# Optimization experiments

Measured on AMD Instinct MI355X. Metric: run time of the kernel, lower is better.

The kernel has to match this reference:

```python
import jax, jax.numpy as jnp
import numpy as np

LMAX = 3
NUM_IRREPS = (LMAX + 1) ** 2  # 16
# Allowed CG paths (l1, l2, l3): triangle inequality, l3 <= LMAX, parity-even (Gaunt-nonzero)
PATHS = tuple((l1, l2, l3)
              for l1 in range(LMAX + 1)
              for l2 in range(LMAX + 1)
              for l3 in range(abs(l1 - l2), min(l1 + l2, LMAX) + 1)
              if (l1 + l2 + l3) % 2 == 0)
NUM_PATHS = len(PATHS)  # 23


def _sph_harm(v, xp):
    """Real spherical harmonics up to l=3 for unit vectors v[..., 3] -> [..., 16]."""
    x, y, z = v[..., 0], v[..., 1], v[..., 2]
    x2, y2, z2 = x * x, y * y, z * z
    Y = [xp.full_like(x, 0.28209479177387814),
         0.4886025119029199 * y, 0.4886025119029199 * z, 0.4886025119029199 * x,
         1.0925484305920792 * x * y, 1.0925484305920792 * y * z,
         0.31539156525252005 * (3.0 * z2 - 1.0),
         1.0925484305920792 * x * z, 0.5462742152960396 * (x2 - y2),
         0.5900435899266435 * y * (3.0 * x2 - y2), 2.890611442640554 * x * y * z,
         0.4570457994644658 * y * (5.0 * z2 - 1.0), 0.3731763325901154 * z * (5.0 * z2 - 3.0),
         0.4570457994644658 * x * (5.0 * z2 - 1.0), 1.445305721320277 * z * (x2 - y2),
         0.5900435899266435 * x * (x2 - 3.0 * y2)]
    return xp.stack(Y, axis=-1)


def _gaunt_coeffs():
    """Gaunt coefficients C[i,j,k] = integral Y_i Y_j Y_k dOmega via exact quadrature."""
    nodes, w = np.polynomial.legendre.leggauss(16)  # cos(theta), exact to deg 31
    nphi = 32
    phi = (np.arange(nphi) + 0.5) * (2.0 * np.pi / nphi)
    ct = nodes[:, None]
    st = np.sqrt(1.0 - ct ** 2)
    dirs = np.stack([st * np.cos(phi), st * np.sin(phi),
                     np.broadcast_to(ct, (16, nphi))], axis=-1).reshape(-1, 3)
    ww = (w[:, None] * np.full((1, nphi), 2.0 * np.pi / nphi)).reshape(-1)
    Y = _sph_harm(dirs, np)  # [M, 16]
    C = np.einsum('m,mi,mj,mk->ijk', ww, Y, Y, Y)
    return C.astype(np.float32)


def setup_inputs() -> dict:
    key = jax.random.key(0)
    k1, k2, k3, k4, k5 = jax.random.split(key, 5)
    N_ATOMS, N_EDGES, HIDDEN, OUT = 20000, 100000, 64, 64
    node_features = jax.random.normal(k1, (N_ATOMS, HIDDEN, NUM_IRREPS), dtype=jnp.float32)
    ev = jax.random.normal(k2, (N_EDGES, 3), dtype=jnp.float32)
    edge_vectors = ev / jnp.linalg.norm(ev, axis=-1, keepdims=True)  # unit directions
    edge_index = jax.random.randint(k3, (2, N_EDGES), 0, N_ATOMS, dtype=jnp.int32)
    cg = jnp.asarray(_gaunt_coeffs())  # [16, 16, 16]
    tp_weights = jax.random.normal(k4, (NUM_PATHS, HIDDEN, OUT), dtype=jnp.float32) / np.sqrt(HIDDEN)
    W_lin = jax.random.normal(k5, (OUT, OUT * NUM_IRREPS), dtype=jnp.float32) / np.sqrt(OUT * NUM_IRREPS)
    b_lin = jnp.zeros((OUT,), dtype=jnp.float32)
    return {"node_features": node_features, "edge_vectors": edge_vectors,
            "edge_index": edge_index, "cg": cg, "tp_weights": tp_weights,
            "W_lin": W_lin, "b_lin": b_lin}


def reference(node_features, edge_vectors, edge_index, cg, tp_weights, W_lin, b_lin):
    n_atoms = node_features.shape[0]
    n_edges = edge_vectors.shape[0]
    out_ch = tp_weights.shape[2]
    Y = _sph_harm(edge_vectors, jnp)                       # [E, 16]
    src = node_features[edge_index[0]]                     # gather: [E, H, 16]
    msgs = jnp.zeros((n_edges, out_ch, NUM_IRREPS), node_features.dtype)
    for p, (l1, l2, l3) in enumerate(PATHS):               # fixed 23-path structural loop
        s1 = slice(l1 * l1, (l1 + 1) ** 2)
        s2 = slice(l2 * l2, (l2 + 1) ** 2)
        s3 = slice(l3 * l3, (l3 + 1) ** 2)
        # CG contraction of node irrep l1 with SH irrep l2 into output irrep l3
        u = jnp.einsum('ehi,ej,ijk->ehk', src[:, :, s1], Y[:, s2], cg[s1, s2, s3])
        msgs = msgs.at[:, :, s3].add(jnp.einsum('ehk,ho->eok', u, tp_weights[p]))
    agg = jax.ops.segment_sum(msgs, edge_index[1], num_segments=n_atoms)  # scatter-add [N, O, 16]
    flat = agg.reshape(n_atoms, -1)
    return flat @ W_lin.T + b_lin
```

## Files before the change

### kernel.cpp

```cpp
#include <hip/hip_runtime.h>


#define NKK 99
#define NKPAD 112
#define EPB 32
#define THREADS 256
#define SA_ESTR 516
#define SU_HSTR 40
#define SU_ESTR 648
#define RED_ESTR 68

typedef _Float16 f16;
typedef f16 f16x4 __attribute__((ext_vector_type(4)));
typedef f16 f16x8 __attribute__((ext_vector_type(8)));
typedef float f32x4 __attribute__((ext_vector_type(4)));

__device__ __constant__ short PK_P[NKK] = {
  0, 1,1,1, 2,2,2,2,2, 3,3,3,3,3,3,3, 4,4,4, 5, 6,6,6,6,6, 7,7,7,
  8,8,8,8,8,8,8, 9,9,9,9,9, 10,10,10,10,10, 11,11,11, 12,12,12,12,12,12,12,
  13, 14,14,14,14,14, 15,15,15, 16,16,16,16,16,16,16, 17,17,17,17,17,17,17,
  18,18,18,18,18, 19,19,19, 20,20,20,20,20,20,20, 21, 22,22,22,22,22};
__device__ __constant__ short KK_L1[NKK] = {
  0, 0,0,0, 0,0,0,0,0, 0,0,0,0,0,0,0, 1,1,1, 1, 1,1,1,1,1, 1,1,1,
  1,1,1,1,1,1,1, 1,1,1,1,1, 2,2,2,2,2, 2,2,2, 2,2,2,2,2,2,2,
  2, 2,2,2,2,2, 2,2,2, 2,2,2,2,2,2,2, 3,3,3,3,3,3,3,
  3,3,3,3,3, 3,3,3, 3,3,3,3,3,3,3, 3, 3,3,3,3,3};
__device__ __constant__ short KK_L2[NKK] = {
  0, 1,1,1, 2,2,2,2,2, 3,3,3,3,3,3,3, 0,0,0, 1, 1,1,1,1,1, 2,2,2,
  2,2,2,2,2,2,2, 3,3,3,3,3, 0,0,0,0,0, 1,1,1, 1,1,1,1,1,1,1,
  2, 2,2,2,2,2, 3,3,3, 3,3,3,3,3,3,3, 0,0,0,0,0,0,0,
  1,1,1,1,1, 2,2,2, 2,2,2,2,2,2,2, 3, 3,3,3,3,3};
__device__ __constant__ short KK_KG[NKK] = {
  0, 1,2,3, 4,5,6,7,8, 9,10,11,12,13,14,15, 1,2,3, 0, 4,5,6,7,8, 1,2,3,
  9,10,11,12,13,14,15, 4,5,6,7,8, 4,5,6,7,8, 1,2,3, 9,10,11,12,13,14,15,
  0, 4,5,6,7,8, 1,2,3, 9,10,11,12,13,14,15, 9,10,11,12,13,14,15,
  4,5,6,7,8, 1,2,3, 9,10,11,12,13,14,15, 0, 4,5,6,7,8};

__global__ __launch_bounds__(256) void compute_F(const float* __restrict__ tpw,
                                                 const float* __restrict__ wlin,
                                                 const float* __restrict__ cg,
                                                 f16* __restrict__ F,
                                                 f16* __restrict__ CGd) {
  int kk = blockIdx.x;
  int tid = threadIdx.x;

  {
    int i = tid >> 4, j = tid & 15;
    f16 v = (f16)0.f;
    if (kk < NKK) {
      int l1 = KK_L1[kk], l2 = KK_L2[kk], kg = KK_KG[kk];
      int b1 = l1 * l1, b2 = l2 * l2;
      if (i >= b1 && i < b1 + 2 * l1 + 1 && j >= b2 && j < b2 + 2 * l2 + 1)
        v = (f16)cg[(i * 16 + j) * 16 + kg];
    }
    CGd[kk * 256 + tid] = v;
  }

  if (kk >= NKK) {
    for (int r = tid; r < 64 * 64; r += 256) F[(size_t)r * NKPAD + kk] = (f16)0.f;
    return;
  }
  int p  = PK_P[kk];
  int c3 = KK_KG[kk];

  __shared__ float wl[64][65];
  for (int idx = tid; idx < 64 * 64; idx += 256) {
    int o2 = idx >> 6, o = idx & 63;
    wl[o2][o] = wlin[o2 * 1024 + o * 16 + c3];
  }
  __syncthreads();

  int h = tid & 63, og = tid >> 6;
  float acc[16];
#pragma unroll
  for (int m = 0; m < 16; ++m) acc[m] = 0.f;
  const float* tw = tpw + (p * 64 + h) * 64;
  for (int o = 0; o < 64; ++o) {
    float w = tw[o];
#pragma unroll
    for (int m = 0; m < 16; ++m) acc[m] += w * wl[og * 16 + m][o];
  }
#pragma unroll
  for (int m = 0; m < 16; ++m)
    F[(size_t)(h * 64 + og * 16 + m) * NKPAD + kk] = (f16)acc[m];
}

__global__ void init_out(float* __restrict__ out, const float* __restrict__ b, int n) {
  int i = blockIdx.x * 256 + threadIdx.x;
  if (i < n) out[i] = b[i & 63];
}

__global__ __launch_bounds__(THREADS, 2) void edge_kernel(
    const float* __restrict__ nf, const float* __restrict__ ev,
    const int* __restrict__ eidx, const f16* __restrict__ CGd,
    const f16* __restrict__ F, float* __restrict__ out, int NE) {

  __shared__ f16 sYh[EPB * 16];
  __shared__ int sSrcA[EPB];
  __shared__ int sDst[EPB];
  __shared__ f16 sA[EPB * SA_ESTR];
  __shared__ f16 sU[EPB * SU_ESTR];

  int tid = threadIdx.x;
  int wave = tid >> 6, lane = tid & 63;
  int lm = lane & 15, lq = lane >> 4;

  if (tid < EPB) {
    int eg = blockIdx.x * EPB + tid;
    int sa = 0, da = -1;
    float x = 0.f, y = 0.f, z = 0.f;
    if (eg < NE) {
      sa = eidx[eg];
      da = eidx[NE + eg];
      x = ev[3 * eg + 0]; y = ev[3 * eg + 1]; z = ev[3 * eg + 2];
    }
    sSrcA[tid] = sa;
    sDst[tid] = da;
    float x2 = x * x, y2 = y * y, z2 = z * z;
    float Y[16];
    Y[0]  = 0.28209479177387814f;
    Y[1]  = 0.4886025119029199f * y;
    Y[2]  = 0.4886025119029199f * z;
    Y[3]  = 0.4886025119029199f * x;
    Y[4]  = 1.0925484305920792f * x * y;
    Y[5]  = 1.0925484305920792f * y * z;
    Y[6]  = 0.31539156525252005f * (3.0f * z2 - 1.0f);
    Y[7]  = 1.0925484305920792f * x * z;
    Y[8]  = 0.5462742152960396f * (x2 - y2);
    Y[9]  = 0.5900435899266435f * y * (3.0f * x2 - y2);
    Y[10] = 2.890611442640554f * x * y * z;
    Y[11] = 0.4570457994644658f * y * (5.0f * z2 - 1.0f);
    Y[12] = 0.3731763325901154f * z * (5.0f * z2 - 3.0f);
    Y[13] = 0.4570457994644658f * x * (5.0f * z2 - 1.0f);
    Y[14] = 1.445305721320277f  * z * (x2 - y2);
    Y[15] = 0.5900435899266435f * x * (x2 - 3.0f * y2);
#pragma unroll
    for (int j = 0; j < 16; ++j) sYh[tid * 16 + j] = (f16)Y[j];
  }
  __syncthreads();

  f16x4 Sf[8][4];
  int ebase = wave * 8;
#pragma unroll
  for (int ei = 0; ei < 8; ++ei) {
    const float4* src4 = (const float4*)nf + (size_t)sSrcA[ebase + ei] * 256;
#pragma unroll
    for (int hg = 0; hg < 4; ++hg) {
      float4 v = src4[(hg * 16 + lm) * 4 + lq];
      Sf[ei][hg] = f16x4{(f16)v.x, (f16)v.y, (f16)v.z, (f16)v.w};
    }
  }

  f16x4 bY0 = *(const f16x4*)&sYh[lm * 16 + lq * 4];
  f16x4 bY1 = *(const f16x4*)&sYh[(16 + lm) * 16 + lq * 4];

  f32x4 acc[2][4];
#pragma unroll
  for (int et = 0; et < 2; ++et)
#pragma unroll
    for (int ot = 0; ot < 4; ++ot) acc[et][ot] = f32x4{0.f, 0.f, 0.f, 0.f};

#define A_BUILD(kkb_, NT_)                                                             \
  {                                                                                    \
    _Pragma("unroll")                                                                  \
    for (int tl = 0; tl < (NT_); ++tl) {                                               \
      int t = wave * (NT_) + tl;                                                       \
      f16x4 aCG = *(const f16x4*)&CGd[(size_t)((kkb_) + t) * 256 + lm * 16 + lq * 4];  \
      f32x4 d0 = __builtin_amdgcn_mfma_f32_16x16x16f16(aCG, bY0, f32x4{0.f, 0.f, 0.f, 0.f}, 0, 0, 0); \
      f32x4 d1 = __builtin_amdgcn_mfma_f32_16x16x16f16(aCG, bY1, f32x4{0.f, 0.f, 0.f, 0.f}, 0, 0, 0); \
      f16x4 dh0 = {(f16)d0[0], (f16)d0[1], (f16)d0[2], (f16)d0[3]};                    \
      f16x4 dh1 = {(f16)d1[0], (f16)d1[1], (f16)d1[2], (f16)d1[3]};                    \
      *(f16x4*)&sA[lm * SA_ESTR + t * 16 + lq * 4] = dh0;         \
      *(f16x4*)&sA[(16 + lm) * SA_ESTR + t * 16 + lq * 4] = dh1;  \
    }                                                                                  \
  }

  A_BUILD(0, 8);
  __syncthreads();

  for (int kg = 0; kg < 3; ++kg) {
#pragma unroll
    for (int hg = 0; hg < 4; ++hg) {
      f16x8 bF[4][4];
#pragma unroll
      for (int hi = 0; hi < 4; ++hi) {
        const f16* Fb = F + (size_t)(hg * 16 + wave + 4 * hi) * 64 * NKPAD + kg * 32 + lq * 8;
#pragma unroll
        for (int ot = 0; ot < 4; ++ot)
          bF[hi][ot] = *(const f16x8*)&Fb[(size_t)(ot * 16 + lm) * NKPAD];
      }

#pragma unroll
      for (int ei = 0; ei < 8; ++ei) {
        int e = ebase + ei;
        f16x4 bS = Sf[ei][hg];
#pragma unroll
        for (int kt = 0; kt < 2; ++kt) {
          f16x4 aA = *(const f16x4*)&sA[e * SA_ESTR + (kt * 16 + lm) * 16 + lq * 4];
          f32x4 d = __builtin_amdgcn_mfma_f32_16x16x16f16(aA, bS, f32x4{0.f, 0.f, 0.f, 0.f}, 0, 0, 0);
          f16x4 dh = {(f16)d[0], (f16)d[1], (f16)d[2], (f16)d[3]};
          *(f16x4*)&sU[e * SU_ESTR + lm * SU_HSTR + kt * 16 + lq * 4] = dh;
        }
      }
      __syncthreads();

#pragma unroll
      for (int hi = 0; hi < 4; ++hi) {
        int hl = wave + 4 * hi;
#pragma unroll
        for (int et = 0; et < 2; ++et) {
          f16x8 a0 = *(const f16x8*)&sU[(size_t)(et * 16 + lm) * SU_ESTR + hl * SU_HSTR + lq * 8];
#pragma unroll
          for (int ot = 0; ot < 4; ++ot)
            acc[et][ot] = __builtin_amdgcn_mfma_f32_16x16x32_f16(a0, bF[hi][ot], acc[et][ot], 0, 0, 0);
        }
      }

      if (hg == 3) {
        __builtin_amdgcn_sched_barrier(0);
        if (kg < 2) A_BUILD((kg + 1) * 32, 8)
        else        A_BUILD(96, 4)
      }
      __syncthreads();
    }
  }

#pragma unroll
  for (int hg = 0; hg < 4; ++hg) {
    f16x4 bFt[4][4];
#pragma unroll
    for (int hi = 0; hi < 4; ++hi) {
      const f16* Fb = F + (size_t)(hg * 16 + wave + 4 * hi) * 64 * NKPAD + 96 + lq * 4;
#pragma unroll
      for (int ot = 0; ot < 4; ++ot)
        bFt[hi][ot] = *(const f16x4*)&Fb[(size_t)(ot * 16 + lm) * NKPAD];
    }

#pragma unroll
    for (int ei = 0; ei < 8; ++ei) {
      int e = ebase + ei;
      f16x4 bS = Sf[ei][hg];
      f16x4 aA = *(const f16x4*)&sA[e * SA_ESTR + lm * 16 + lq * 4];
      f32x4 d = __builtin_amdgcn_mfma_f32_16x16x16f16(aA, bS, f32x4{0.f, 0.f, 0.f, 0.f}, 0, 0, 0);
      f16x4 dh = {(f16)d[0], (f16)d[1], (f16)d[2], (f16)d[3]};
      *(f16x4*)&sU[e * SU_ESTR + lm * SU_HSTR + lq * 4] = dh;
    }
    __syncthreads();

#pragma unroll
    for (int hi = 0; hi < 4; ++hi) {
      int hl = wave + 4 * hi;
#pragma unroll
      for (int et = 0; et < 2; ++et) {
        f16x4 a0 = *(const f16x4*)&sU[(size_t)(et * 16 + lm) * SU_ESTR + hl * SU_HSTR + lq * 4];
#pragma unroll
        for (int ot = 0; ot < 4; ++ot)
          acc[et][ot] = __builtin_amdgcn_mfma_f32_16x16x16f16(a0, bFt[hi][ot], acc[et][ot], 0, 0, 0);
      }
    }
    __syncthreads();
  }

  float* red = (float*)sU;
#pragma unroll
  for (int et = 0; et < 2; ++et)
#pragma unroll
    for (int ot = 0; ot < 4; ++ot)
#pragma unroll
      for (int r = 0; r < 4; ++r) {
        int e = et * 16 + lq * 4 + r;
        int o2 = ot * 16 + lm;
        red[(wave * EPB + e) * RED_ESTR + o2] = acc[et][ot][r];
      }
  __syncthreads();

#pragma unroll
  for (int rep = 0; rep < 8; ++rep) {
    int idx = tid + rep * 256;
    int e = idx >> 6, o2 = idx & 63;
    float s = red[(0 * EPB + e) * RED_ESTR + o2]
            + red[(1 * EPB + e) * RED_ESTR + o2]
            + red[(2 * EPB + e) * RED_ESTR + o2]
            + red[(3 * EPB + e) * RED_ESTR + o2];
    int da = sDst[e];
    if (da >= 0) unsafeAtomicAdd(out + (size_t)da * 64 + o2, s);
  }
}

extern "C" void kernel_launch(void* const* d_in, const int* in_sizes, int n_in,
                              void* d_out, int out_size, void* d_ws, size_t ws_size,
                              hipStream_t stream) {
  const float* nf   = (const float*)d_in[0];
  const float* ev   = (const float*)d_in[1];
  const int*   eidx = (const int*)d_in[2];
  const float* cg   = (const float*)d_in[3];
  const float* tpw  = (const float*)d_in[4];
  const float* wlin = (const float*)d_in[5];
  const float* blin = (const float*)d_in[6];
  float* out = (float*)d_out;

  int NA = in_sizes[0] / 1024;
  int NE = in_sizes[1] / 3;
  f16* F   = (f16*)d_ws;
  f16* CGd = (f16*)((char*)d_ws + (size_t)64 * 64 * NKPAD * 2);

  compute_F<<<NKPAD, 256, 0, stream>>>(tpw, wlin, cg, F, CGd);
  init_out<<<(NA * 64 + 255) / 256, 256, 0, stream>>>(out, blin, NA * 64);
  edge_kernel<<<(NE + EPB - 1) / EPB, THREADS, 0, stream>>>(nf, ev, eidx, CGd, F, out, NE);
}
```

Before: 447.2 us.

## Stream source node features per h-group with register prefetch instead of preloading

```diff
diff --git a/kernel.cpp b/kernel.cpp
--- a/kernel.cpp
+++ b/kernel.cpp
@@ -139,17 +139,15 @@
   }
   __syncthreads();
 
-  f16x4 Sf[8][4];
   int ebase = wave * 8;
-#pragma unroll
-  for (int ei = 0; ei < 8; ++ei) {
-    const float4* src4 = (const float4*)nf + (size_t)sSrcA[ebase + ei] * 256;
-#pragma unroll
-    for (int hg = 0; hg < 4; ++hg) {
-      float4 v = src4[(hg * 16 + lm) * 4 + lq];
-      Sf[ei][hg] = f16x4{(f16)v.x, (f16)v.y, (f16)v.z, (f16)v.w};
-    }
-  }
+  int srcAtom[8];
+#pragma unroll
+  for (int ei = 0; ei < 8; ++ei) srcAtom[ei] = sSrcA[ebase + ei];
+
+  float4 SfN4[8];
+#pragma unroll
+  for (int ei = 0; ei < 8; ++ei)
+    SfN4[ei] = ((const float4*)nf)[(size_t)srcAtom[ei] * 256 + (0 * 16 + lm) * 4 + lq];
 
   f16x4 bY0 = *(const f16x4*)&sYh[lm * 16 + lq * 4];
   f16x4 bY1 = *(const f16x4*)&sYh[(16 + lm) * 16 + lq * 4];
@@ -181,6 +179,13 @@
   for (int kg = 0; kg < 3; ++kg) {
 #pragma unroll
     for (int hg = 0; hg < 4; ++hg) {
+      f16x4 SfC[8];
+#pragma unroll
+      for (int ei = 0; ei < 8; ++ei) {
+        float4 v = SfN4[ei];
+        SfC[ei] = f16x4{(f16)v.x, (f16)v.y, (f16)v.z, (f16)v.w};
+      }
+
       f16x8 bF[4][4];
 #pragma unroll
       for (int hi = 0; hi < 4; ++hi) {
@@ -193,7 +198,7 @@
 #pragma unroll
       for (int ei = 0; ei < 8; ++ei) {
         int e = ebase + ei;
-        f16x4 bS = Sf[ei][hg];
+        f16x4 bS = SfC[ei];
 #pragma unroll
         for (int kt = 0; kt < 2; ++kt) {
           f16x4 aA = *(const f16x4*)&sA[e * SA_ESTR + (kt * 16 + lm) * 16 + lq * 4];
@@ -204,8 +209,9 @@
       }
       __syncthreads();
 
-#pragma unroll
-      for (int hi = 0; hi < 4; ++hi) {
+      __builtin_amdgcn_s_setprio(1);
+#pragma unroll
+      for (int hi = 0; hi < 2; ++hi) {
         int hl = wave + 4 * hi;
 #pragma unroll
         for (int et = 0; et < 2; ++et) {
@@ -215,6 +221,28 @@
             acc[et][ot] = __builtin_amdgcn_mfma_f32_16x16x32_f16(a0, bF[hi][ot], acc[et][ot], 0, 0, 0);
         }
       }
+      __builtin_amdgcn_s_setprio(0);
+
+      {
+        int nhg = (hg + 1) & 3;
+#pragma unroll
+        for (int ei = 0; ei < 8; ++ei)
+          SfN4[ei] = ((const float4*)nf)[(size_t)srcAtom[ei] * 256 + (nhg * 16 + lm) * 4 + lq];
+      }
+
+      __builtin_amdgcn_s_setprio(1);
+#pragma unroll
+      for (int hi = 2; hi < 4; ++hi) {
+        int hl = wave + 4 * hi;
+#pragma unroll
+        for (int et = 0; et < 2; ++et) {
+          f16x8 a0 = *(const f16x8*)&sU[(size_t)(et * 16 + lm) * SU_ESTR + hl * SU_HSTR + lq * 8];
+#pragma unroll
+          for (int ot = 0; ot < 4; ++ot)
+            acc[et][ot] = __builtin_amdgcn_mfma_f32_16x16x32_f16(a0, bF[hi][ot], acc[et][ot], 0, 0, 0);
+        }
+      }
+      __builtin_amdgcn_s_setprio(0);
 
       if (hg == 3) {
         __builtin_amdgcn_sched_barrier(0);
@@ -227,6 +255,13 @@
 
 #pragma unroll
   for (int hg = 0; hg < 4; ++hg) {
+    f16x4 SfC[8];
+#pragma unroll
+    for (int ei = 0; ei < 8; ++ei) {
+      float4 v = SfN4[ei];
+      SfC[ei] = f16x4{(f16)v.x, (f16)v.y, (f16)v.z, (f16)v.w};
+    }
+
     f16x4 bFt[4][4];
 #pragma unroll
     for (int hi = 0; hi < 4; ++hi) {
@@ -239,7 +274,7 @@
 #pragma unroll
     for (int ei = 0; ei < 8; ++ei) {
       int e = ebase + ei;
-      f16x4 bS = Sf[ei][hg];
+      f16x4 bS = SfC[ei];
       f16x4 aA = *(const f16x4*)&sA[e * SA_ESTR + lm * 16 + lq * 4];
       f32x4 d = __builtin_amdgcn_mfma_f32_16x16x16f16(aA, bS, f32x4{0.f, 0.f, 0.f, 0.f}, 0, 0, 0);
       f16x4 dh = {(f16)d[0], (f16)d[1], (f16)d[2], (f16)d[3]};
@@ -247,8 +282,9 @@
     }
     __syncthreads();
 
-#pragma unroll
-    for (int hi = 0; hi < 4; ++hi) {
+    __builtin_amdgcn_s_setprio(1);
+#pragma unroll
+    for (int hi = 0; hi < 2; ++hi) {
       int hl = wave + 4 * hi;
 #pragma unroll
       for (int et = 0; et < 2; ++et) {
@@ -258,6 +294,28 @@
           acc[et][ot] = __builtin_amdgcn_mfma_f32_16x16x16f16(a0, bFt[hi][ot], acc[et][ot], 0, 0, 0);
       }
     }
+    __builtin_amdgcn_s_setprio(0);
+
+    if (hg < 3) {
+      int nhg = hg + 1;
+#pragma unroll
+      for (int ei = 0; ei < 8; ++ei)
+        SfN4[ei] = ((const float4*)nf)[(size_t)srcAtom[ei] * 256 + (nhg * 16 + lm) * 4 + lq];
+    }
+
+    __builtin_amdgcn_s_setprio(1);
+#pragma unroll
+    for (int hi = 2; hi < 4; ++hi) {
+      int hl = wave + 4 * hi;
+#pragma unroll
+      for (int et = 0; et < 2; ++et) {
+        f16x4 a0 = *(const f16x4*)&sU[(size_t)(et * 16 + lm) * SU_ESTR + hl * SU_HSTR + lq * 4];
+#pragma unroll
+        for (int ot = 0; ot < 4; ++ot)
+          acc[et][ot] = __builtin_amdgcn_mfma_f32_16x16x16f16(a0, bFt[hi][ot], acc[et][ot], 0, 0, 0);
+      }
+    }
+    __builtin_amdgcn_s_setprio(0);
     __syncthreads();
   }
 
```

New measurement: 612.5 us. 1.37x slower.
